# Kernel tuning notes

Measured on AMD Instinct MI355X. Metric: run time of the kernel, lower is better.

The kernel has to match this reference:

```python
import jax, jax.numpy as jnp
import numpy as np
import math

B, S, D, H, R = 4, 4096, 1024, 16, 256
DK = D // H

def setup_inputs() -> dict:
    key = jax.random.key(0)
    ks = jax.random.split(key, 16)
    def lin(k, fan_in, fan_out):
        # torch Linear default init: U(-1/sqrt(fan_in), 1/sqrt(fan_in))
        bound = 1.0 / math.sqrt(fan_in)
        kw, kb = jax.random.split(k)
        W = jax.random.uniform(kw, (fan_out, fan_in), jnp.float32, -bound, bound)
        b = jax.random.uniform(kb, (fan_out,), jnp.float32, -bound, bound)
        return W, b
    Wq, bq = lin(ks[0], D, D)
    Wk, bk = lin(ks[1], D, D)
    Wv, bv = lin(ks[2], D, D)
    Wo, bo = lin(ks[3], D, D)
    # xavier_uniform over last two dims (S, R)
    xav = math.sqrt(6.0 / (S + R))
    E = jax.random.uniform(ks[4], (H, S, R), jnp.float32, -xav, xav)
    F = jax.random.uniform(ks[5], (H, S, R), jnp.float32, -xav, xav)
    query = jax.random.normal(ks[6], (B, S, D), jnp.float32)
    key_ = jax.random.normal(ks[7], (B, S, D), jnp.float32)
    value = jax.random.normal(ks[8], (B, S, D), jnp.float32)
    return {"query": query, "key": key_, "value": value,
            "Wq": Wq, "bq": bq, "Wk": Wk, "bk": bk, "Wv": Wv, "bv": bv,
            "Wo": Wo, "bo": bo, "E": E, "F": F}

def _split_heads(x):
    # [B, S, D] -> [B, H, S, DK]
    b, s, _ = x.shape
    return x.reshape(b, s, H, DK).transpose(0, 2, 1, 3)

def reference(query, key, value, Wq, bq, Wk, bk, Wv, bv, Wo, bo, E, F):
    q = _split_heads(query @ Wq.T + bq)   # [B,H,S,DK]
    k = _split_heads(key @ Wk.T + bk)
    v = _split_heads(value @ Wv.T + bv)
    # key^T @ E : [B,H,DK,S] @ [H,S,R] -> [B,H,DK,R]
    kp = jnp.einsum('bhsd,hsr->bhdr', k, E)
    vp = jnp.einsum('bhsd,hsr->bhdr', v, F)
    attn = jnp.einsum('bhsd,bhdr->bhsr', q, kp) / math.sqrt(DK)
    attn = jax.nn.softmax(attn, axis=-1)  # [B,H,S,R]
    out = jnp.einsum('bhsr,bhdr->bhsd', attn, vp)  # [B,H,S,DK]
    out = out.transpose(0, 2, 1, 3).reshape(query.shape[0], -1, D)
    return out @ Wo.T + bo
```

## Files before the change

kernel.cpp:

```cpp
#include <hip/hip_runtime.h>


typedef __bf16 bf16;
typedef bf16 bf16x8 __attribute__((ext_vector_type(8)));
typedef bf16 bf16x4 __attribute__((ext_vector_type(4)));
typedef float f32x4 __attribute__((ext_vector_type(4)));

constexpr int BB = 4, SS = 4096, DD = 1024, HH = 16, RR = 256, DK = 64;

#define QSCALE 0.1803368801111204f

__device__ __forceinline__ void gl2lds16(const void* g, void* l, int lane)
{
#if __has_builtin(__builtin_amdgcn_global_load_lds)
    auto gp = reinterpret_cast<const __attribute__((address_space(1))) void*>(
        reinterpret_cast<uintptr_t>(g));
    auto lp = reinterpret_cast<__attribute__((address_space(3))) void*>(
        reinterpret_cast<uintptr_t>(l));
    __builtin_amdgcn_global_load_lds(gp, lp, 16, 0, 0);
    (void)lane;
#else
    *(bf16x8*)((char*)l + lane * 16) = *(const bf16x8*)g;
#endif
}

#define VMW6  asm volatile("s_waitcnt vmcnt(6)" ::: "memory")
#define VMW0  asm volatile("s_waitcnt vmcnt(0)" ::: "memory")
#define LGKM0 asm volatile("s_waitcnt lgkmcnt(0)" ::: "memory")

__global__ void cvt_f32_bf16(const float* __restrict__ in, bf16* __restrict__ out, int n)
{
    int i = (blockIdx.x * 256 + threadIdx.x) * 8;
    if (i < n) {
        float4 v0 = *(const float4*)(in + i);
        float4 v1 = *(const float4*)(in + i + 4);
        bf16x8 h;
        h[0] = (bf16)v0.x; h[1] = (bf16)v0.y; h[2] = (bf16)v0.z; h[3] = (bf16)v0.w;
        h[4] = (bf16)v1.x; h[5] = (bf16)v1.y; h[6] = (bf16)v1.z; h[7] = (bf16)v1.w;
        *(bf16x8*)(out + i) = h;
    }
}

__global__ void transpose_cvt(const float* __restrict__ in, bf16* __restrict__ out,
                              int rows, int cols)
{
    __shared__ float t[64][65];
    const float* I = in + (size_t)blockIdx.z * rows * cols;
    bf16* O = out + (size_t)blockIdx.z * rows * cols;
    int c0 = blockIdx.x * 64, r0 = blockIdx.y * 64;
    int tx = threadIdx.x, ty = threadIdx.y;
#pragma unroll
    for (int i = ty; i < 64; i += 4)
        t[i][tx] = I[(size_t)(r0 + i) * cols + c0 + tx];
    __syncthreads();
#pragma unroll
    for (int i = ty; i < 64; i += 4)
        O[(size_t)(c0 + i) * rows + r0 + tx] = (bf16)t[tx][i];
}

template <bool OUT_F32>
__global__ __launch_bounds__(512, 2) void gemm_bt(const bf16* __restrict__ A,
                                                  const bf16* __restrict__ W,
                                                  const float* __restrict__ bias,
                                                  void* __restrict__ Cp,
                                                  int M, int N, int K, float oscale)
{
    __shared__ bf16 As[2][256][64];
    __shared__ bf16 Bs[2][256][64];
    const int tid = threadIdx.x, wv = tid >> 6, lane = tid & 63;
    const int g = lane >> 4, lr = lane & 15;

    const int nwg = gridDim.x;
    const int cpx = nwg >> 3;
    const int bid = blockIdx.x;
    const int swz = (bid & 7) * cpx + (bid >> 3);
    const int gx = N >> 8;
    const int mt = swz / gx, nt = swz % gx;
    const int m0 = mt * 256, n0 = nt * 256;
    const int wm = (wv >> 2) * 128, wn = (wv & 3) * 64;

    const int lrow8 = lane >> 3;
    const int gcol = ((lane & 7) ^ lrow8) * 8;

    f32x4 acc[8][4] = {};
    bf16x8 bF[4][2];

    auto stageA = [&](int buf, int tk, int h) {
#pragma unroll
        for (int s2 = 0; s2 < 2; ++s2) {
            int j = wv + s2 * 8;
            int rb = h * 64 + (j >> 3) * 128 + (j & 7) * 8;
            gl2lds16(A + (size_t)(m0 + rb + lrow8) * 1024 + tk * 64 + gcol,
                     &As[buf][rb][0], lane);
        }
    };
    auto stageB = [&](int buf, int tk, int h) {
#pragma unroll
        for (int s2 = 0; s2 < 2; ++s2) {
            int j = wv + s2 * 8;
            int rb = h * 32 + (j >> 2) * 64 + (j & 3) * 8;
            gl2lds16(W + (size_t)(n0 + rb + lrow8) * 1024 + tk * 64 + gcol,
                     &Bs[buf][rb][0], lane);
        }
    };

#define PH(PB, MH, LOADB, STAGE_STMT, VM_STMT)                                   \
    {                                                                            \
        bf16x8 aF[4][2];                                                         \
        _Pragma("unroll") for (int mm = 0; mm < 4; ++mm) {                       \
            _Pragma("unroll") for (int kk = 0; kk < 2; ++kk) {                   \
                aF[mm][kk] = *(const bf16x8*)((const char*)&As[PB][wm + MH * 64 + mm * 16 + lr][0] \
                              + (((kk * 4 + g) ^ (lr & 7)) << 4)); } }           \
        if (LOADB) {                                                             \
            _Pragma("unroll") for (int j = 0; j < 4; ++j) {                      \
                _Pragma("unroll") for (int kk = 0; kk < 2; ++kk) {               \
                    bF[j][kk] = *(const bf16x8*)((const char*)&Bs[PB][wn + j * 16 + lr][0] \
                                  + (((kk * 4 + g) ^ (lr & 7)) << 4)); } }       \
        }                                                                        \
        STAGE_STMT;                                                              \
        VM_STMT;                                                                 \
        __builtin_amdgcn_s_barrier();                                            \
        LGKM0;                                                                   \
        __builtin_amdgcn_sched_barrier(0);                                       \
        __builtin_amdgcn_s_setprio(1);                                           \
        _Pragma("unroll") for (int kk = 0; kk < 2; ++kk) {                       \
            _Pragma("unroll") for (int mm = 0; mm < 4; ++mm) {                   \
                _Pragma("unroll") for (int j = 0; j < 4; ++j) {                  \
                    acc[MH * 4 + mm][j] = __builtin_amdgcn_mfma_f32_16x16x32_bf16( \
                        aF[mm][kk], bF[j][kk], acc[MH * 4 + mm][j], 0, 0, 0); } } } \
        __builtin_amdgcn_s_setprio(0);                                           \
        __builtin_amdgcn_s_barrier();                                            \
    }

    stageA(0, 0, 0); stageA(0, 0, 1); stageB(0, 0, 0); stageB(0, 0, 1);
    stageB(1, 1, 0); stageB(1, 1, 1); stageA(1, 1, 0);
    VMW6;
    __builtin_amdgcn_s_barrier();

#pragma unroll 1
    for (int t = 0; t < 13; t += 2) {
        PH(0, 0, true,  { stageA(1, t + 1, 1); }, (void)0);
        PH(0, 1, false, { stageB(0, t + 2, 0); stageB(0, t + 2, 1); stageA(0, t + 2, 0); }, VMW6);
        PH(1, 0, true,  { stageA(0, t + 2, 1); }, (void)0);
        PH(1, 1, false, { stageB(1, t + 3, 0); stageB(1, t + 3, 1); stageA(1, t + 3, 0); }, VMW6);
    }
    PH(0, 0, true,  { stageA(1, 15, 1); }, (void)0);
    PH(0, 1, false, (void)0, VMW0);
    PH(1, 0, true,  (void)0, (void)0);
    PH(1, 1, false, (void)0, (void)0);
#undef PH

    float bv[4];
#pragma unroll
    for (int n = 0; n < 4; ++n) bv[n] = bias[n0 + wn + n * 16 + lr];

    if constexpr (OUT_F32) {
#pragma unroll
        for (int n = 0; n < 4; ++n) {
            int col = n0 + wn + n * 16 + lr;
#pragma unroll
            for (int m = 0; m < 8; ++m) {
                int row = m0 + wm + m * 16 + 4 * g;
#pragma unroll
                for (int i = 0; i < 4; ++i)
                    ((float*)Cp)[(size_t)(row + i) * N + col] = (acc[m][n][i] + bv[n]) * oscale;
            }
        }
    } else {
        bf16* myb = (wv < 4) ? (&As[0][0][0] + wv * 8192)
                             : (&Bs[0][0][0] + (wv - 4) * 8192);
#pragma unroll
        for (int m = 0; m < 8; ++m)
#pragma unroll
            for (int n = 0; n < 4; ++n) {
                int colb = n * 32 + lr * 2;
#pragma unroll
                for (int i = 0; i < 4; ++i) {
                    int row = m * 16 + 4 * g + i;
                    *(bf16*)((char*)myb + row * 128 + (colb ^ ((row & 7) << 4))) =
                        (bf16)((acc[m][n][i] + bv[n]) * oscale);
                }
            }
        __builtin_amdgcn_wave_barrier();
        bf16* Cb = (bf16*)Cp + (size_t)(m0 + wm) * N + n0 + wn;
#pragma unroll
        for (int it = 0; it < 16; ++it) {
            int r = it * 8 + lrow8;
            int sl = lane & 7;
            bf16x8 vv = *(const bf16x8*)((const char*)myb + r * 128 + ((sl ^ (r & 7)) << 4));
            *(bf16x8*)(Cb + (size_t)r * N + sl * 8) = vv;
        }
    }
}

__global__ __launch_bounds__(256) void kpvp_gemm(const bf16* __restrict__ X,
                                                 const bf16* __restrict__ P,
                                                 float* __restrict__ out)
{
    __shared__ bf16 Ak[64][40];
    __shared__ bf16 Bs[256][32];
    const int b = blockIdx.z, h = blockIdx.y;
    const int s0 = blockIdx.x * 512;
    const int tid = threadIdx.x, wv = tid >> 6, lane = tid & 63;
    const int g = lane >> 4, lr = lane & 15;
    const int lrow = lane >> 2, lcol = (lane & 3) * 8;
    const bf16* Pg = P + ((size_t)h * RR + wv * 64 + lrow) * SS + lcol;
    f32x4 acc[4][4] = {};

    for (int kt = 0; kt < 512; kt += 32) {
        const int sb = s0 + kt;
        __syncthreads();
#pragma unroll
        for (int j = 0; j < 4; ++j)
            gl2lds16(Pg + (size_t)(j * 16) * SS + sb, &Bs[wv * 64 + j * 16][0], lane);
        {
            int sl = tid >> 3, dblk = (tid & 7) * 8;
            bf16x8 v = *(const bf16x8*)(X + ((size_t)b * SS + sb + sl) * DD + h * DK + dblk);
#pragma unroll
            for (int j = 0; j < 8; ++j) Ak[dblk + j][sl] = v[j];
        }
        __syncthreads();

        bf16x8 a[4], bb[4];
#pragma unroll
        for (int m = 0; m < 4; ++m) a[m] = *(const bf16x8*)&Ak[m * 16 + lr][g * 8];
#pragma unroll
        for (int n = 0; n < 4; ++n) bb[n] = *(const bf16x8*)&Bs[wv * 64 + n * 16 + lr][g * 8];
#pragma unroll
        for (int m = 0; m < 4; ++m)
#pragma unroll
            for (int n = 0; n < 4; ++n)
                acc[m][n] = __builtin_amdgcn_mfma_f32_16x16x32_bf16(a[m], bb[n], acc[m][n], 0, 0, 0);
    }

    float* o = out + ((size_t)(b * HH + h)) * DK * RR;
#pragma unroll
    for (int m = 0; m < 4; ++m)
#pragma unroll
        for (int n = 0; n < 4; ++n) {
            int r = wv * 64 + n * 16 + lr;
#pragma unroll
            for (int i = 0; i < 4; ++i)
                atomicAdd(o + (size_t)(m * 16 + 4 * g + i) * RR + r, acc[m][n][i]);
        }
}

__global__ __launch_bounds__(512) void attn_fused(const bf16* __restrict__ qb,
                                                  const bf16* __restrict__ kpt,
                                                  const bf16* __restrict__ vpb,
                                                  bf16* __restrict__ ctx)
{
    __shared__ bf16 KPs[256][72];
    __shared__ bf16 VPs[64][264];
    __shared__ bf16 Ps[8][16][264];
    const int b = blockIdx.z, h = blockIdx.y, qt = blockIdx.x;
    const int tid = threadIdx.x, wv = tid >> 6, lane = tid & 63;
    const int g = lane >> 4, lr = lane & 15;
    const bf16* kph = kpt + ((size_t)(b * HH + h)) * RR * DK;
    const bf16* vph = vpb + ((size_t)(b * HH + h)) * DK * RR;

#pragma unroll
    for (int p = 0; p < 4; ++p) {
        int f = p * 512 + tid;
        *(bf16x8*)&KPs[f >> 3][(f & 7) * 8] = *(const bf16x8*)(kph + (size_t)f * 8);
        *(bf16x8*)&VPs[f >> 5][(f & 31) * 8] = *(const bf16x8*)(vph + (size_t)f * 8);
    }

    const bf16* qbase = qb + (size_t)b * SS * DD + h * DK;
    int row0 = qt * 1024 + wv * 16;
    bf16x8 aq0 = *(const bf16x8*)(qbase + (size_t)(row0 + lr) * DD + g * 8);
    bf16x8 aq1 = *(const bf16x8*)(qbase + (size_t)(row0 + lr) * DD + 32 + g * 8);
    __syncthreads();

    for (int it = 0; it < 8; ++it) {
        f32x4 acc[16] = {};
        __builtin_amdgcn_s_setprio(1);
#pragma unroll
        for (int nf = 0; nf < 16; ++nf) {
            bf16x8 b0 = *(const bf16x8*)&KPs[nf * 16 + lr][g * 8];
            bf16x8 b1 = *(const bf16x8*)&KPs[nf * 16 + lr][32 + g * 8];
            acc[nf] = __builtin_amdgcn_mfma_f32_16x16x32_bf16(aq0, b0, acc[nf], 0, 0, 0);
            acc[nf] = __builtin_amdgcn_mfma_f32_16x16x32_bf16(aq1, b1, acc[nf], 0, 0, 0);
        }
        __builtin_amdgcn_s_setprio(0);

        bf16x8 aqn0 = aq0, aqn1 = aq1;
        if (it < 7) {
            const bf16* qr = qbase + (size_t)(row0 + 128 + lr) * DD;
            aqn0 = *(const bf16x8*)(qr + g * 8);
            aqn1 = *(const bf16x8*)(qr + 32 + g * 8);
        }

        float rs[4];
#pragma unroll
        for (int i = 0; i < 4; ++i) {
            float s = 0.f;
#pragma unroll
            for (int nf = 0; nf < 16; ++nf) {
                float pv = exp2f(acc[nf][i]);
                acc[nf][i] = pv;
                s += pv;
            }
#pragma unroll
            for (int msk = 1; msk < 16; msk <<= 1) s += __shfl_xor(s, msk, 64);
            rs[i] = 1.f / s;
        }

#pragma unroll
        for (int nf = 0; nf < 16; ++nf)
#pragma unroll
            for (int i = 0; i < 4; ++i)
                Ps[wv][4 * g + i][nf * 16 + lr] = (bf16)acc[nf][i];
        __builtin_amdgcn_wave_barrier();

        f32x4 o[4] = {};
        __builtin_amdgcn_s_setprio(1);
#pragma unroll
        for (int ks = 0; ks < 8; ++ks) {
            bf16x8 pa = *(const bf16x8*)&Ps[wv][lr][ks * 32 + g * 8];
#pragma unroll
            for (int n = 0; n < 4; ++n) {
                bf16x8 vb = *(const bf16x8*)&VPs[n * 16 + lr][ks * 32 + g * 8];
                o[n] = __builtin_amdgcn_mfma_f32_16x16x32_bf16(pa, vb, o[n], 0, 0, 0);
            }
        }
        __builtin_amdgcn_s_setprio(0);
        __builtin_amdgcn_wave_barrier();

#pragma unroll
        for (int n = 0; n < 4; ++n)
#pragma unroll
            for (int i = 0; i < 4; ++i)
                Ps[wv][4 * g + i][n * 16 + lr] = (bf16)(o[n][i] * rs[i]);
        __builtin_amdgcn_wave_barrier();
        bf16* crow = ctx + (size_t)(b * SS + row0) * DD + h * DK;
#pragma unroll
        for (int p = 0; p < 2; ++p) {
            int r = p * 8 + (lane >> 3), c = (lane & 7) * 8;
            bf16x8 ov = *(const bf16x8*)&Ps[wv][r][c];
            *(bf16x8*)(crow + (size_t)r * DD + c) = ov;
        }
        __builtin_amdgcn_wave_barrier();

        aq0 = aqn0; aq1 = aqn1;
        row0 += 128;
    }
}

extern "C" void kernel_launch(void* const* d_in, const int* in_sizes, int n_in,
                              void* d_out, int out_size, void* d_ws, size_t ws_size,
                              hipStream_t stream)
{
    const float* query = (const float*)d_in[0];
    const float* key   = (const float*)d_in[1];
    const float* value = (const float*)d_in[2];
    const float* Wq = (const float*)d_in[3];  const float* bq = (const float*)d_in[4];
    const float* Wk = (const float*)d_in[5];  const float* bk = (const float*)d_in[6];
    const float* Wv = (const float*)d_in[7];  const float* bv = (const float*)d_in[8];
    const float* Wo = (const float*)d_in[9];  const float* bo = (const float*)d_in[10];
    const float* E  = (const float*)d_in[11];
    const float* F  = (const float*)d_in[12];

    char* w = (char*)d_ws;
    size_t off = 0;
    auto alloc = [&](size_t bytes) -> char* {
        char* p = w + off;
        off += (bytes + 255) & ~(size_t)255;
        return p;
    };

    const size_t DW   = (size_t)DD * DD;
    const size_t BSD  = (size_t)BB * SS * DD;
    const size_t HRS  = (size_t)HH * RR * SS;
    const size_t BHDR = (size_t)BB * HH * DK * RR;

    bf16* wqb = (bf16*)alloc(DW * 2);
    bf16* wkb = (bf16*)alloc(DW * 2);
    bf16* wvb = (bf16*)alloc(DW * 2);
    bf16* wob = (bf16*)alloc(DW * 2);
    bf16* ebt = (bf16*)alloc(HRS * 2);
    bf16* fbt = (bf16*)alloc(HRS * 2);
    bf16* qin = (bf16*)alloc(BSD * 2);
    bf16* kin = (bf16*)alloc(BSD * 2);
    bf16* vin = (bf16*)alloc(BSD * 2);
    bf16* qbuf = (bf16*)alloc(BSD * 2);
    bf16* kbuf = (bf16*)alloc(BSD * 2);
    bf16* vbuf = (bf16*)alloc(BSD * 2);
    if (off > ws_size) return;

    float* kpf  = (float*)qin;
    float* vpf  = kpf + BHDR;
    bf16*  kpt  = (bf16*)kin;
    bf16*  vpbb = kpt + BHDR;
    bf16*  ctx  = (bf16*)vin;

    cvt_f32_bf16<<<(int)(DW / 2048), 256, 0, stream>>>(Wq, wqb, (int)DW);
    cvt_f32_bf16<<<(int)(DW / 2048), 256, 0, stream>>>(Wk, wkb, (int)DW);
    cvt_f32_bf16<<<(int)(DW / 2048), 256, 0, stream>>>(Wv, wvb, (int)DW);
    cvt_f32_bf16<<<(int)(DW / 2048), 256, 0, stream>>>(Wo, wob, (int)DW);
    cvt_f32_bf16<<<(int)(BSD / 2048), 256, 0, stream>>>(query, qin, (int)BSD);
    cvt_f32_bf16<<<(int)(BSD / 2048), 256, 0, stream>>>(key,   kin, (int)BSD);
    cvt_f32_bf16<<<(int)(BSD / 2048), 256, 0, stream>>>(value, vin, (int)BSD);

    dim3 tb(64, 4);
    transpose_cvt<<<dim3(RR / 64, SS / 64, HH), tb, 0, stream>>>(E, ebt, SS, RR);
    transpose_cvt<<<dim3(RR / 64, SS / 64, HH), tb, 0, stream>>>(F, fbt, SS, RR);

    const int nwg = ((BB * SS) / 256) * (DD / 256);
    gemm_bt<false><<<nwg, 512, 0, stream>>>(qin, wqb, bq, qbuf, BB * SS, DD, DD, QSCALE);
    gemm_bt<false><<<nwg, 512, 0, stream>>>(kin, wkb, bk, kbuf, BB * SS, DD, DD, 1.0f);
    gemm_bt<false><<<nwg, 512, 0, stream>>>(vin, wvb, bv, vbuf, BB * SS, DD, DD, 1.0f);

    hipMemsetAsync(kpf, 0, BHDR * 4 * 2, stream);
    kpvp_gemm<<<dim3(SS / 512, HH, BB), 256, 0, stream>>>(kbuf, ebt, kpf);
    kpvp_gemm<<<dim3(SS / 512, HH, BB), 256, 0, stream>>>(vbuf, fbt, vpf);

    transpose_cvt<<<dim3(RR / 64, DK / 64, BB * HH), tb, 0, stream>>>(kpf, kpt, DK, RR);
    cvt_f32_bf16<<<(int)(BHDR / 2048), 256, 0, stream>>>(vpf, vpbb, (int)BHDR);

    attn_fused<<<dim3(SS / 1024, HH, BB), 512, 0, stream>>>(qbuf, kpt, vpbb, ctx);

    gemm_bt<true><<<nwg, 512, 0, stream>>>(ctx, wob, bo, d_out, BB * SS, DD, DD, 1.0f);
}
```

Before: 426.4 us.

## Shrink GEMM tiles to 256x128 with BK=32 and four waves-per-SIMD occupancy

Reworks the projection GEMM from a 256x256 tile with K-step 64 and a four-phase pipeline to a 256x128 tile with K-step 32 and a simple double-buffered loop. Each of the 8 waves now computes a 64x64 block. LDS use drops to 48 KB and launch bounds target 4 blocks per CU, doubling the grid to 512 workgroups. This aims at better CU fill and latency hiding, but lowers arithmetic intensity per tile and doubles the number of barriers per K.

Result: slower. 445.6 us (+4.5%).

```diff
diff --git a/kernel.cpp b/kernel.cpp
--- a/kernel.cpp
+++ b/kernel.cpp
@@ -24,7 +24,7 @@
 #endif
 }
 
-#define VMW6  asm volatile("s_waitcnt vmcnt(6)" ::: "memory")
+#define VMW3  asm volatile("s_waitcnt vmcnt(3)" ::: "memory")
 #define VMW0  asm volatile("s_waitcnt vmcnt(0)" ::: "memory")
 #define LGKM0 asm volatile("s_waitcnt lgkmcnt(0)" ::: "memory")
 
@@ -59,14 +59,14 @@
 }
 
 template <bool OUT_F32>
-__global__ __launch_bounds__(512, 2) void gemm_bt(const bf16* __restrict__ A,
+__global__ __launch_bounds__(512, 4) void gemm_bt(const bf16* __restrict__ A,
                                                   const bf16* __restrict__ W,
                                                   const float* __restrict__ bias,
                                                   void* __restrict__ Cp,
                                                   int M, int N, int K, float oscale)
 {
-    __shared__ bf16 As[2][256][64];
-    __shared__ bf16 Bs[2][256][64];
+    __shared__ bf16 As[2][256][32];
+    __shared__ bf16 Bs[2][128][32];
     const int tid = threadIdx.x, wv = tid >> 6, lane = tid & 63;
     const int g = lane >> 4, lr = lane & 15;
 
@@ -74,81 +74,64 @@
     const int cpx = nwg >> 3;
     const int bid = blockIdx.x;
     const int swz = (bid & 7) * cpx + (bid >> 3);
-    const int gx = N >> 8;
+    const int gx = N >> 7;
     const int mt = swz / gx, nt = swz % gx;
-    const int m0 = mt * 256, n0 = nt * 256;
-    const int wm = (wv >> 2) * 128, wn = (wv & 3) * 64;
-
-    const int lrow8 = lane >> 3;
-    const int gcol = ((lane & 7) ^ lrow8) * 8;
-
-    f32x4 acc[8][4] = {};
-    bf16x8 bF[4][2];
-
-    auto stageA = [&](int buf, int tk, int h) {
+    const int m0 = mt * 256, n0 = nt * 128;
+    const int wm = (wv >> 1) * 64, wn = (wv & 1) * 64;
+
+    const int srow = lane >> 2;
+    const int scol = ((lane & 3) ^ ((lane >> 4) & 3)) * 8;
+
+    f32x4 acc[4][4] = {};
+
+    auto stageA = [&](int buf, int tk) {
 #pragma unroll
         for (int s2 = 0; s2 < 2; ++s2) {
-            int j = wv + s2 * 8;
-            int rb = h * 64 + (j >> 3) * 128 + (j & 7) * 8;
-            gl2lds16(A + (size_t)(m0 + rb + lrow8) * 1024 + tk * 64 + gcol,
-                     &As[buf][rb][0], lane);
+            int c = wv * 2 + s2;
+            gl2lds16(A + (size_t)(m0 + c * 16 + srow) * 1024 + tk * 32 + scol,
+                     &As[buf][c * 16][0], lane);
         }
     };
-    auto stageB = [&](int buf, int tk, int h) {
-#pragma unroll
-        for (int s2 = 0; s2 < 2; ++s2) {
-            int j = wv + s2 * 8;
-            int rb = h * 32 + (j >> 2) * 64 + (j & 3) * 8;
-            gl2lds16(W + (size_t)(n0 + rb + lrow8) * 1024 + tk * 64 + gcol,
-                     &Bs[buf][rb][0], lane);
-        }
+    auto stageB = [&](int buf, int tk) {
+        gl2lds16(W + (size_t)(n0 + wv * 16 + srow) * 1024 + tk * 32 + scol,
+                 &Bs[buf][wv * 16][0], lane);
     };
 
-#define PH(PB, MH, LOADB, STAGE_STMT, VM_STMT)                                   \
+#define PHK(PB, STAGE_STMT, VM_STMT)                                             \
     {                                                                            \
-        bf16x8 aF[4][2];                                                         \
-        _Pragma("unroll") for (int mm = 0; mm < 4; ++mm) {                       \
-            _Pragma("unroll") for (int kk = 0; kk < 2; ++kk) {                   \
-                aF[mm][kk] = *(const bf16x8*)((const char*)&As[PB][wm + MH * 64 + mm * 16 + lr][0] \
-                              + (((kk * 4 + g) ^ (lr & 7)) << 4)); } }           \
-        if (LOADB) {                                                             \
-            _Pragma("unroll") for (int j = 0; j < 4; ++j) {                      \
-                _Pragma("unroll") for (int kk = 0; kk < 2; ++kk) {               \
-                    bF[j][kk] = *(const bf16x8*)((const char*)&Bs[PB][wn + j * 16 + lr][0] \
-                                  + (((kk * 4 + g) ^ (lr & 7)) << 4)); } }       \
-        }                                                                        \
-        STAGE_STMT;                                                              \
-        VM_STMT;                                                                 \
-        __builtin_amdgcn_s_barrier();                                            \
+        const int so = (g ^ (lr >> 2)) << 4;                                     \
+        bf16x8 aF[4], bF[4];                                                     \
+        _Pragma("unroll") for (int mm = 0; mm < 4; ++mm)                         \
+            aF[mm] = *(const bf16x8*)((const char*)&As[PB][wm + mm * 16 + lr][0] + so); \
+        _Pragma("unroll") for (int nn = 0; nn < 4; ++nn)                         \
+            bF[nn] = *(const bf16x8*)((const char*)&Bs[PB][wn + nn * 16 + lr][0] + so); \
         LGKM0;                                                                   \
+        __builtin_amdgcn_s_barrier();                 \
+        STAGE_STMT;                                     \
+        VM_STMT;                                             \
+        __builtin_amdgcn_s_barrier();                   \
         __builtin_amdgcn_sched_barrier(0);                                       \
         __builtin_amdgcn_s_setprio(1);                                           \
-        _Pragma("unroll") for (int kk = 0; kk < 2; ++kk) {                       \
-            _Pragma("unroll") for (int mm = 0; mm < 4; ++mm) {                   \
-                _Pragma("unroll") for (int j = 0; j < 4; ++j) {                  \
-                    acc[MH * 4 + mm][j] = __builtin_amdgcn_mfma_f32_16x16x32_bf16( \
-                        aF[mm][kk], bF[j][kk], acc[MH * 4 + mm][j], 0, 0, 0); } } } \
+        _Pragma("unroll") for (int mm = 0; mm < 4; ++mm) {                       \
+            _Pragma("unroll") for (int nn = 0; nn < 4; ++nn) {                   \
+                acc[mm][nn] = __builtin_amdgcn_mfma_f32_16x16x32_bf16(           \
+                    aF[mm], bF[nn], acc[mm][nn], 0, 0, 0); } }                   \
         __builtin_amdgcn_s_setprio(0);                                           \
-        __builtin_amdgcn_s_barrier();                                            \
-    }
-
-    stageA(0, 0, 0); stageA(0, 0, 1); stageB(0, 0, 0); stageB(0, 0, 1);
-    stageB(1, 1, 0); stageB(1, 1, 1); stageA(1, 1, 0);
-    VMW6;
+    }
+
+    stageA(0, 0); stageB(0, 0);
+    stageA(1, 1); stageB(1, 1);
+    VMW3;
     __builtin_amdgcn_s_barrier();
 
 #pragma unroll 1
-    for (int t = 0; t < 13; t += 2) {
-        PH(0, 0, true,  { stageA(1, t + 1, 1); }, (void)0);
-        PH(0, 1, false, { stageB(0, t + 2, 0); stageB(0, t + 2, 1); stageA(0, t + 2, 0); }, VMW6);
-        PH(1, 0, true,  { stageA(0, t + 2, 1); }, (void)0);
-        PH(1, 1, false, { stageB(1, t + 3, 0); stageB(1, t + 3, 1); stageA(1, t + 3, 0); }, VMW6);
-    }
-    PH(0, 0, true,  { stageA(1, 15, 1); }, (void)0);
-    PH(0, 1, false, (void)0, VMW0);
-    PH(1, 0, true,  (void)0, (void)0);
-    PH(1, 1, false, (void)0, (void)0);
-#undef PH
+    for (int t = 0; t < 30; ++t) {
+        const int pb = t & 1;
+        PHK(pb, { stageA(pb, t + 2); stageB(pb, t + 2); }, VMW3);
+    }
+    PHK(0, (void)0, VMW0);
+    PHK(1, (void)0, (void)0);
+#undef PHK
 
     float bv[4];
 #pragma unroll
@@ -159,7 +142,7 @@
         for (int n = 0; n < 4; ++n) {
             int col = n0 + wn + n * 16 + lr;
 #pragma unroll
-            for (int m = 0; m < 8; ++m) {
+            for (int m = 0; m < 4; ++m) {
                 int row = m0 + wm + m * 16 + 4 * g;
 #pragma unroll
                 for (int i = 0; i < 4; ++i)
@@ -167,28 +150,31 @@
             }
         }
     } else {
-        bf16* myb = (wv < 4) ? (&As[0][0][0] + wv * 8192)
-                             : (&Bs[0][0][0] + (wv - 4) * 8192);
-#pragma unroll
-        for (int m = 0; m < 8; ++m)
-#pragma unroll
-            for (int n = 0; n < 4; ++n) {
-                int colb = n * 32 + lr * 2;
-#pragma unroll
-                for (int i = 0; i < 4; ++i) {
-                    int row = m * 16 + 4 * g + i;
-                    *(bf16*)((char*)myb + row * 128 + (colb ^ ((row & 7) << 4))) =
-                        (bf16)((acc[m][n][i] + bv[n]) * oscale);
+        char* myb = (char*)&As[0][0][0] + wv * 4096;
+#pragma unroll
+        for (int mh = 0; mh < 2; ++mh) {
+#pragma unroll
+            for (int mm = 0; mm < 2; ++mm)
+#pragma unroll
+                for (int n = 0; n < 4; ++n) {
+                    int colb = (n * 16 + lr) * 2;
+#pragma unroll
+                    for (int i = 0; i < 4; ++i) {
+                        int row = mm * 16 + 4 * g + i;
+                        *(bf16*)(myb + row * 128 + (colb ^ ((row & 7) << 4))) =
+                            (bf16)((acc[mh * 2 + mm][n][i] + bv[n]) * oscale);
+                    }
                 }
+            __builtin_amdgcn_wave_barrier();
+            bf16* Cb = (bf16*)Cp + (size_t)(m0 + wm + mh * 32) * N + n0 + wn;
+#pragma unroll
+            for (int it = 0; it < 4; ++it) {
+                int r = it * 8 + (lane >> 3);
+                int sl = lane & 7;
+                bf16x8 vv = *(const bf16x8*)(myb + r * 128 + ((sl ^ (r & 7)) << 4));
+                *(bf16x8*)(Cb + (size_t)r * N + sl * 8) = vv;
             }
-        __builtin_amdgcn_wave_barrier();
-        bf16* Cb = (bf16*)Cp + (size_t)(m0 + wm) * N + n0 + wn;
-#pragma unroll
-        for (int it = 0; it < 16; ++it) {
-            int r = it * 8 + lrow8;
-            int sl = lane & 7;
-            bf16x8 vv = *(const bf16x8*)((const char*)myb + r * 128 + ((sl ^ (r & 7)) << 4));
-            *(bf16x8*)(Cb + (size_t)r * N + sl * 8) = vv;
+            __builtin_amdgcn_wave_barrier();
         }
     }
 }
@@ -406,7 +392,7 @@
     transpose_cvt<<<dim3(RR / 64, SS / 64, HH), tb, 0, stream>>>(E, ebt, SS, RR);
     transpose_cvt<<<dim3(RR / 64, SS / 64, HH), tb, 0, stream>>>(F, fbt, SS, RR);
 
-    const int nwg = ((BB * SS) / 256) * (DD / 256);
+    const int nwg = ((BB * SS) / 256) * (DD / 128);
     gemm_bt<false><<<nwg, 512, 0, stream>>>(qin, wqb, bq, qbuf, BB * SS, DD, DD, QSCALE);
     gemm_bt<false><<<nwg, 512, 0, stream>>>(kin, wkb, bk, kbuf, BB * SS, DD, DD, 1.0f);
     gemm_bt<false><<<nwg, 512, 0, stream>>>(vin, wvb, bv, vbuf, BB * SS, DD, DD, 1.0f);
```
